# Kernel optimization log

Hardware: AMD Instinct MI355X
Metric: run time of the kernel (lower is better)

The kernel has to match this reference:

```python
import jax, jax.numpy as jnp
import numpy as np

D_MODEL = 1024
D_STATE = 32
EXPAND = 2
D_INNER = D_MODEL * EXPAND
B_SZ = 2
SEQ = 512


def setup_inputs() -> dict:
    key = jax.random.key(0)
    ks = jax.random.split(key, 10)
    x = jax.random.normal(ks[0], (B_SZ, SEQ, D_MODEL), dtype=jnp.float32)
    W_in = jax.random.normal(ks[1], (2 * D_INNER, D_MODEL), dtype=jnp.float32) * 0.02
    A_log = jax.random.uniform(ks[2], (D_INNER, D_STATE), minval=-4.0, maxval=-1.0, dtype=jnp.float32)
    W_B = jax.random.normal(ks[3], (D_STATE, D_MODEL), dtype=jnp.float32) * 0.02
    W_C = jax.random.normal(ks[4], (D_STATE, D_MODEL), dtype=jnp.float32) * 0.02
    W_dt = jax.random.normal(ks[5], (D_INNER, D_MODEL), dtype=jnp.float32) * 0.02
    b_dt = jnp.zeros((D_INNER,), dtype=jnp.float32)
    dt_bias = jnp.zeros((D_INNER,), dtype=jnp.float32) - 4.0
    rope_freq = jax.random.normal(ks[6], (D_STATE // 2,), dtype=jnp.float32) * 0.01
    ln_w = jnp.ones((D_INNER,), dtype=jnp.float32)
    ln_b = jnp.zeros((D_INNER,), dtype=jnp.float32)
    W_out = jax.random.normal(ks[7], (D_MODEL, D_INNER), dtype=jnp.float32) * 0.02
    return {"x": x, "W_in": W_in, "A_log": A_log, "W_B": W_B, "W_C": W_C,
            "W_dt": W_dt, "b_dt": b_dt, "dt_bias": dt_bias, "rope_freq": rope_freq,
            "ln_w": ln_w, "ln_b": ln_b, "W_out": W_out}


def _forward(x, W_in, A_log, W_B, W_C, W_dt, b_dt, dt_bias, rope_freq, ln_w, ln_b, W_out):
    B, L, _ = x.shape
    half = D_STATE // 2
    offset = 0

    xz = jnp.einsum('bld,ed->ble', x, W_in)                 # [B,L,2*D_INNER]
    x_inner = xz[..., :D_INNER]                             # [B,L,DI]
    z = jax.nn.silu(xz[..., D_INNER:])                      # [B,L,DI]

    A = -jnp.exp(A_log)                                     # [DI,DS]
    Bm = jnp.einsum('bld,nd->bln', x, W_B)                  # [B,L,DS]
    Cm = jnp.einsum('bld,nd->bln', x, W_C)                  # [B,L,DS]
    dt = jax.nn.softplus(jnp.einsum('bld,ed->ble', x, W_dt) + b_dt + dt_bias)  # [B,L,DI]

    # trapezoidal discretization
    dtA = dt[..., None] * A                                 # [B,L,DI,DS]
    denom = 1.0 - dtA / 2.0
    A_bar = (1.0 + dtA / 2.0) / denom                       # [B,L,DI,DS]
    B_bar = dt[..., None] / denom                           # [B,L,DI,DS]

    # per-step rope rotation angles: angle_t = rope_freq * (t + offset)
    t_idx = jnp.arange(L, dtype=jnp.float32) + offset       # [L]
    ang = t_idx[:, None] * rope_freq                        # [L,half]
    cos_a = jnp.cos(ang)
    sin_a = jnp.sin(ang)

    def step(state, inp):
        A_t, Bb_t, B_t, x_t, C_t, c_t, s_t = inp
        # state update: [B,DI,DS]
        state = A_t * state + Bb_t * B_t[:, None, :] * x_t[:, :, None]
        real = state[..., :half]
        imag = state[..., half:]
        state = jnp.concatenate([real * c_t - imag * s_t,
                                 real * s_t + imag * c_t], axis=-1)
        y_t = jnp.einsum('bds,bs->bd', state, C_t)          # [B,DI]
        return state, y_t

    state0 = jnp.zeros((B, D_INNER, D_STATE), dtype=x.dtype)
    xs = (jnp.swapaxes(A_bar, 0, 1), jnp.swapaxes(B_bar, 0, 1),
          jnp.swapaxes(Bm, 0, 1), jnp.swapaxes(x_inner, 0, 1),
          jnp.swapaxes(Cm, 0, 1), cos_a, sin_a)
    final_state, ys = jax.lax.scan(step, state0, xs)        # ys: [L,B,DI]
    out = jnp.swapaxes(ys, 0, 1) * z                        # [B,L,DI]

    # LayerNorm over last dim (eps=1e-5, torch default)
    mu = jnp.mean(out, axis=-1, keepdims=True)
    var = jnp.mean((out - mu) ** 2, axis=-1, keepdims=True)
    out = (out - mu) * jax.lax.rsqrt(var + 1e-5) * ln_w + ln_b

    out = jnp.einsum('ble,de->bld', out, W_out)             # [B,L,D_MODEL]
    return out, final_state


def reference(x, W_in, A_log, W_B, W_C, W_dt, b_dt, dt_bias, rope_freq, ln_w, ln_b, W_out):
    return _forward(x, W_in, A_log, W_B, W_C, W_dt, b_dt, dt_bias, rope_freq, ln_w, ln_b, W_out)
```

## Files before the change

### kernel.cpp

```cpp
#include <hip/hip_runtime.h>
#include <math.h>

#define B_SZ 2
#define SEQ 512
#define DM 1024
#define DI 2048
#define DS 32
#define TOK (B_SZ*SEQ)
#define NCH 8
#define CLEN (SEQ/NCH)
#define NPAIRH 32768

#define NFUSED 6272

typedef float v2f __attribute__((ext_vector_type(2)));

__device__ __forceinline__ unsigned short f2bf(float f) {
  unsigned int u = __builtin_bit_cast(unsigned int, f);
  unsigned int r = u + 0x7fffu + ((u >> 16) & 1u);
  return (unsigned short)(r >> 16);
}

template<int CTRL>
__device__ __forceinline__ float row_ror_add(float x) {
  int s = __builtin_amdgcn_update_dpp(0, __builtin_bit_cast(int, x), CTRL, 0xf, 0xf, false);
  return x + __builtin_bit_cast(float, s);
}
__device__ __forceinline__ float row16_sum(float v) {
  v = row_ror_add<0x121>(v);
  v = row_ror_add<0x122>(v);
  v = row_ror_add<0x124>(v);
  v = row_ror_add<0x128>(v);
  return v;
}

__global__ __launch_bounds__(256) void fused_cast(const float* __restrict__ x,
                                                  const float* __restrict__ W_in,
                                                  const float* __restrict__ W_dt,
                                                  const float* __restrict__ W_B,
                                                  const float* __restrict__ W_C,
                                                  const float* __restrict__ W_out,
                                                  unsigned short* __restrict__ xb,
                                                  unsigned short* __restrict__ wcat,
                                                  unsigned short* __restrict__ wob) {
  int g = blockIdx.x * 256 + threadIdx.x;
  const float* s; unsigned short* dd; int off;
  if      (g <  131072) { s = x;     dd = xb;             off = 0; }
  else if (g <  655360) { s = W_in;  dd = wcat;           off = 131072; }
  else if (g <  917504) { s = W_dt;  dd = wcat + 4194304; off = 655360; }
  else if (g <  921600) { s = W_B;   dd = wcat + 6291456; off = 917504; }
  else if (g <  925696) { s = W_C;   dd = wcat + 6324224; off = 921600; }
  else if (g < 1187840) { s = W_out; dd = wob;            off = 925696; }
  else return;
  int i = g - off;
  float4 a = ((const float4*)s)[i * 2];
  float4 b = ((const float4*)s)[i * 2 + 1];
  union { unsigned short us[8]; uint4 v; } o;
  o.us[0] = f2bf(a.x); o.us[1] = f2bf(a.y); o.us[2] = f2bf(a.z); o.us[3] = f2bf(a.w);
  o.us[4] = f2bf(b.x); o.us[5] = f2bf(b.y); o.us[6] = f2bf(b.z); o.us[7] = f2bf(b.w);
  ((uint4*)dd)[i] = o.v;
}

typedef __attribute__((ext_vector_type(8))) short  frag8;
typedef __attribute__((ext_vector_type(4))) float  facc4;

__device__ __forceinline__ void gload_lds16(const unsigned short* g, unsigned short* l) {
  __builtin_amdgcn_global_load_lds((const __attribute__((address_space(1))) unsigned int*)g,
                                   (__attribute__((address_space(3))) unsigned int*)l, 16, 0, 0);
}
__device__ __forceinline__ void gload_lds16f(const float* g, float* l) {
  __builtin_amdgcn_global_load_lds((const __attribute__((address_space(1))) unsigned int*)g,
                                   (__attribute__((address_space(3))) unsigned int*)l, 16, 0, 0);
}

__device__ __forceinline__ float softplus_fast(float v) {
  return fmaxf(v, 0.f) + __logf(1.f + __expf(-fabsf(v)));
}

template<int MT, int NT, int KSP, bool ROUTE>
__global__ __launch_bounds__(256) void gemm_mfma(const unsigned short* __restrict__ A,
                                                 const unsigned short* __restrict__ Bw,
                                                 int K,
                                                 float* __restrict__ o_xs,
                                                 float* __restrict__ o_zb,
                                                 float* __restrict__ o_dts,
                                                 float* __restrict__ o_bcb,
                                                 const float* __restrict__ b_dt,
                                                 const float* __restrict__ dt_bias,
                                                 float* __restrict__ o_c, int ldc) {
  __shared__ __align__(16) unsigned short As[64 * 64];
  __shared__ __align__(16) unsigned short Bs[64 * 64];
  const int tid = threadIdx.x;
  const int w = tid >> 6, lane = tid & 63;
  const int wm = w >> 1, wn = w & 1;
  const int bid = blockIdx.x;
  const int Wk = (bid & 7) * ((int)gridDim.x >> 3) + (bid >> 3);
  const int ks = Wk / (MT * NT);
  const int rem = Wk % (MT * NT);
  const int m0 = (rem % MT) * 64;
  const int n0 = (rem / MT) * 64;
  const int kLen = K / KSP, kBeg = ks * kLen;
  const int r = lane & 15, q = lane >> 4;
  const int srow = lane >> 3;
  const int scol = ((lane & 7) ^ (srow & 7)) * 8;
  facc4 acc[2][2] = {};
  const unsigned short* Ag = A + (size_t)m0 * K + kBeg;
  const unsigned short* Bg = Bw + (size_t)n0 * K + kBeg;

  for (int k0 = 0; k0 < kLen; k0 += 64) {
#pragma unroll
    for (int k = 0; k < 2; ++k) {
      int ch = w * 2 + k;
      gload_lds16(Ag + (size_t)(ch * 8 + srow) * K + k0 + scol, &As[ch * 512]);
      gload_lds16(Bg + (size_t)(ch * 8 + srow) * K + k0 + scol, &Bs[ch * 512]);
    }
    __syncthreads();
#pragma unroll
    for (int kk = 0; kk < 2; ++kk) {
      frag8 af[2], bf[2];
      const int sw = ((kk * 4 + q) ^ (r & 7)) * 8;
#pragma unroll
      for (int i = 0; i < 2; ++i)
        af[i] = *(const frag8*)&As[(wm * 32 + i * 16 + r) * 64 + sw];
#pragma unroll
      for (int jj = 0; jj < 2; ++jj)
        bf[jj] = *(const frag8*)&Bs[(wn * 32 + jj * 16 + r) * 64 + sw];
#pragma unroll
      for (int i = 0; i < 2; ++i)
#pragma unroll
        for (int jj = 0; jj < 2; ++jj)
          acc[i][jj] = __builtin_amdgcn_mfma_f32_16x16x32_bf16(af[i], bf[jj], acc[i][jj], 0, 0, 0);
    }
    __syncthreads();
  }

#pragma unroll
  for (int i = 0; i < 2; ++i) {
#pragma unroll
    for (int jj = 0; jj < 2; ++jj) {
      int n = n0 + wn * 32 + jj * 16 + r;
      int mb = m0 + wm * 32 + i * 16 + q * 4;
      if (ROUTE) {
        if (n < 2048) {
#pragma unroll
          for (int rg = 0; rg < 4; ++rg)
            o_xs[(size_t)(mb + rg) * DI + n] = acc[i][jj][rg];
        } else if (n < 4096) {
#pragma unroll
          for (int rg = 0; rg < 4; ++rg)
            o_zb[(size_t)(mb + rg) * DI + (n - 2048)] = acc[i][jj][rg];
        } else if (n < 6144) {
          int d = n - 4096;
          float bias = b_dt[d] + dt_bias[d];
#pragma unroll
          for (int rg = 0; rg < 4; ++rg)
            o_dts[(size_t)(mb + rg) * DI + d] = softplus_fast(acc[i][jj][rg] + bias);
        } else if (n < 6176) {
#pragma unroll
          for (int rg = 0; rg < 4; ++rg)
            o_bcb[(size_t)(mb + rg) * DS + (n - 6144)] = acc[i][jj][rg];
        } else if (n < 6208) {
#pragma unroll
          for (int rg = 0; rg < 4; ++rg)
            o_bcb[(size_t)TOK * DS + (size_t)(mb + rg) * DS + (n - 6176)] = acc[i][jj][rg];
        }
      } else {
        float* oc = o_c + (size_t)ks * (MT * 64) * ldc;
#pragma unroll
        for (int rg = 0; rg < 4; ++rg)
          oc[(size_t)(mb + rg) * ldc + n] = acc[i][jj][rg];
      }
    }
  }
}

__global__ __launch_bounds__(256) void addk(const float* __restrict__ p0,
                                            const float* __restrict__ p1,
                                            float* __restrict__ o) {
  int i = blockIdx.x * 256 + threadIdx.x;
  float4 a = ((const float4*)p0)[i];
  float4 b = ((const float4*)p1)[i];
  ((float4*)o)[i] = make_float4(a.x + b.x, a.y + b.y, a.z + b.z, a.w + b.w);
}

__global__ __launch_bounds__(256) void scan_p1(const float* __restrict__ xs,
                                               const float* __restrict__ dts,
                                               const float* __restrict__ bcb,
                                               const float* __restrict__ A_log,
                                               const float* __restrict__ rope,
                                               float* __restrict__ Pbuf) {
  __shared__ __align__(16) float lds[6144];
  const int blk = blockIdx.x;
  const int c = blk >> 7;
  const int sub = blk & 127;
  const int b = sub >> 6;
  const int dbase = (sub & 63) << 5;
  const int tid = threadIdx.x;
  const int wv = tid >> 6, lane = tid & 63;
  const int j = tid & 15;
  const int ca = (tid >> 4) & 15;
  const int l0 = c * CLEN;
  const size_t base = (size_t)(b * SEQ + l0);

  {
    int row = wv * 16 + (lane >> 3);
    int col = (lane & 7) << 2;
#pragma unroll
    for (int k = 0; k < 2; ++k) {
      gload_lds16f(xs  + (base + row + k * 8) * DI + dbase + col, &lds[(wv * 16 + k * 8) * 32]);
      gload_lds16f(dts + (base + row + k * 8) * DI + dbase + col, &lds[2048 + (wv * 16 + k * 8) * 32]);
    }
#pragma unroll
    for (int k = 0; k < 2; ++k) {
      int seg = wv * 2 + k;
      gload_lds16f(bcb + base * DS + seg * 256 + lane * 4, &lds[4096 + seg * 256]);
    }
  }

  const int dA = dbase + 2 * ca;
  v2f Ar, Ai;
  Ar.x = -0.5f * expf(A_log[dA * DS + j]);
  Ar.y = -0.5f * expf(A_log[(dA + 1) * DS + j]);
  Ai.x = -0.5f * expf(A_log[dA * DS + j + 16]);
  Ai.y = -0.5f * expf(A_log[(dA + 1) * DS + j + 16]);
  const float fr = rope[j];
  float sn, cs, sF, cF;
  sincosf((float)l0 * fr, &sn, &cs);
  sincosf(fr, &sF, &cF);
  __syncthreads();

  v2f p00 = {1.f, 1.f}, p01 = {0.f, 0.f}, p10 = {0.f, 0.f}, p11 = {1.f, 1.f};
  v2f ur = {0.f, 0.f}, ui = {0.f, 0.f};

#pragma unroll 4
  for (int tt = 0; tt < CLEN; ++tt) {
    const int ro = tt * 32;
    v2f xin = *(const v2f*)&lds[ro + 2 * ca];
    v2f dtd = *(const v2f*)&lds[2048 + ro + 2 * ca];
    float Br = lds[4096 + ro + j];
    float Bi = lds[4096 + ro + j + 16];
    v2f hr = dtd * Ar, hi = dtd * Ai;
    v2f invr, invi;
    invr.x = __builtin_amdgcn_rcpf(1.f - hr.x);
    invr.y = __builtin_amdgcn_rcpf(1.f - hr.y);
    invi.x = __builtin_amdgcn_rcpf(1.f - hi.x);
    invi.y = __builtin_amdgcn_rcpf(1.f - hi.y);
    v2f Abr = 2.f * invr - 1.f;
    v2f Abi = 2.f * invi - 1.f;
    v2f dx = dtd * xin;
    v2f bxr = dx * invr * Br;
    v2f bxi = dx * invi * Bi;
    v2f tr = Abr * ur + bxr;
    v2f ti = Abi * ui + bxi;
    ur = tr * cs - ti * sn;
    ui = tr * sn + ti * cs;
    v2f q00 = Abr * p00, q01 = Abr * p01;
    v2f q10 = Abi * p10, q11 = Abi * p11;
    p00 = q00 * cs - q10 * sn; p10 = q00 * sn + q10 * cs;
    p01 = q01 * cs - q11 * sn; p11 = q01 * sn + q11 * cs;
    float nc = fmaf(cs, cF, -sn * sF);
    float ns = fmaf(sn, cF,  cs * sF);
    cs = nc; sn = ns;
  }
  const int pc = (b * 1024 + (dbase >> 1) + ca) * 16 + j;
  float2* Pb2 = (float2*)Pbuf;
  Pb2[(c * 6 + 0) * NPAIRH + pc] = make_float2(p00.x, p00.y);
  Pb2[(c * 6 + 1) * NPAIRH + pc] = make_float2(p01.x, p01.y);
  Pb2[(c * 6 + 2) * NPAIRH + pc] = make_float2(p10.x, p10.y);
  Pb2[(c * 6 + 3) * NPAIRH + pc] = make_float2(p11.x, p11.y);
  Pb2[(c * 6 + 4) * NPAIRH + pc] = make_float2(ur.x, ur.y);
  Pb2[(c * 6 + 5) * NPAIRH + pc] = make_float2(ui.x, ui.y);
}

__global__ __launch_bounds__(256) void scan_p3(const float* __restrict__ xs,
                                               const float* __restrict__ dts,
                                               const float* __restrict__ bcb,
                                               const float* __restrict__ A_log,
                                               const float* __restrict__ rope,
                                               const float* __restrict__ Pbuf,
                                               float* __restrict__ y,
                                               float* __restrict__ fstate) {
  __shared__ __align__(16) float lds[8192];
  const int blk = blockIdx.x;
  const int c = blk >> 7;
  const int sub = blk & 127;
  const int b = sub >> 6;
  const int dbase = (sub & 63) << 5;
  const int tid = threadIdx.x;
  const int wv = tid >> 6, lane = tid & 63;
  const int j = tid & 15;
  const int ca = (tid >> 4) & 15;
  const int l0 = c * CLEN;
  const size_t base = (size_t)(b * SEQ + l0);

  {
    int row = wv * 16 + (lane >> 3);
    int col = (lane & 7) << 2;
#pragma unroll
    for (int k = 0; k < 2; ++k) {
      gload_lds16f(xs  + (base + row + k * 8) * DI + dbase + col, &lds[(wv * 16 + k * 8) * 32]);
      gload_lds16f(dts + (base + row + k * 8) * DI + dbase + col, &lds[2048 + (wv * 16 + k * 8) * 32]);
    }
#pragma unroll
    for (int k = 0; k < 2; ++k) {
      int seg = wv * 2 + k;
      gload_lds16f(bcb + base * DS + seg * 256 + lane * 4, &lds[4096 + seg * 256]);
      gload_lds16f(bcb + (size_t)TOK * DS + base * DS + seg * 256 + lane * 4, &lds[6144 + seg * 256]);
    }
  }

  const int dA = dbase + 2 * ca;
  v2f Ar, Ai;
  Ar.x = -0.5f * expf(A_log[dA * DS + j]);
  Ar.y = -0.5f * expf(A_log[(dA + 1) * DS + j]);
  Ai.x = -0.5f * expf(A_log[dA * DS + j + 16]);
  Ai.y = -0.5f * expf(A_log[(dA + 1) * DS + j + 16]);
  const float fr = rope[j];
  float sn, cs, sF, cF;
  sincosf((float)l0 * fr, &sn, &cs);
  sincosf(fr, &sF, &cF);

  const int pc = (b * 1024 + (dbase >> 1) + ca) * 16 + j;
  const float2* Pb2 = (const float2*)Pbuf;
  v2f sr = {0.f, 0.f}, si = {0.f, 0.f};
  for (int k = 0; k < c; ++k) {
    float2 f;
    f = Pb2[(k * 6 + 0) * NPAIRH + pc]; v2f p00 = {f.x, f.y};
    f = Pb2[(k * 6 + 1) * NPAIRH + pc]; v2f p01 = {f.x, f.y};
    f = Pb2[(k * 6 + 2) * NPAIRH + pc]; v2f p10 = {f.x, f.y};
    f = Pb2[(k * 6 + 3) * NPAIRH + pc]; v2f p11 = {f.x, f.y};
    f = Pb2[(k * 6 + 4) * NPAIRH + pc]; v2f ur  = {f.x, f.y};
    f = Pb2[(k * 6 + 5) * NPAIRH + pc]; v2f ui  = {f.x, f.y};
    v2f nr = p00 * sr + p01 * si + ur;
    v2f ni = p10 * sr + p11 * si + ui;
    sr = nr; si = ni;
  }
  __syncthreads();

  float* yp = y + base * DI + dA;

#pragma unroll 4
  for (int tt = 0; tt < CLEN; ++tt) {
    const int ro = tt * 32;
    v2f xin = *(const v2f*)&lds[ro + 2 * ca];
    v2f dtd = *(const v2f*)&lds[2048 + ro + 2 * ca];
    float Br = lds[4096 + ro + j];
    float Bi = lds[4096 + ro + j + 16];
    float Cr = lds[6144 + ro + j];
    float Ci = lds[6144 + ro + j + 16];
    v2f hr = dtd * Ar, hi = dtd * Ai;
    v2f invr, invi;
    invr.x = __builtin_amdgcn_rcpf(1.f - hr.x);
    invr.y = __builtin_amdgcn_rcpf(1.f - hr.y);
    invi.x = __builtin_amdgcn_rcpf(1.f - hi.x);
    invi.y = __builtin_amdgcn_rcpf(1.f - hi.y);
    v2f Abr = 2.f * invr - 1.f;
    v2f Abi = 2.f * invi - 1.f;
    v2f dx = dtd * xin;
    v2f bxr = dx * invr * Br;
    v2f bxi = dx * invi * Bi;
    v2f tr = Abr * sr + bxr;
    v2f ti = Abi * si + bxi;
    sr = tr * cs - ti * sn;
    si = tr * sn + ti * cs;
    v2f p = sr * Cr + si * Ci;
    float pA = row16_sum(p.x);
    float pB = row16_sum(p.y);
    if (j == 0) *(float2*)&yp[tt * DI] = make_float2(pA, pB);
    float nc = fmaf(cs, cF, -sn * sF);
    float ns = fmaf(sn, cF,  cs * sF);
    cs = nc; sn = ns;
  }
  if (c == NCH - 1) {
    fstate[((size_t)b * DI + dA) * DS + j]          = sr.x;
    fstate[((size_t)b * DI + dA) * DS + j + 16]     = si.x;
    fstate[((size_t)b * DI + dA + 1) * DS + j]      = sr.y;
    fstate[((size_t)b * DI + dA + 1) * DS + j + 16] = si.y;
  }
}

__global__ __launch_bounds__(256) void gate_ln(const float* __restrict__ y,
                                               const float* __restrict__ zb,
                                               const float* __restrict__ lw,
                                               const float* __restrict__ lb,
                                               unsigned short* __restrict__ o) {
  int tok = blockIdx.x;
  int t = threadIdx.x;
  float g[8];
  float sum = 0.f, sq = 0.f;
#pragma unroll
  for (int i = 0; i < 8; ++i) {
    int dd = t + i * 256;
    float yv = y[(size_t)tok * DI + dd];
    float zv = zb[(size_t)tok * DI + dd];
    float sg = zv / (1.f + __expf(-zv));
    float v = yv * sg;
    g[i] = v; sum += v; sq += v * v;
  }
#pragma unroll
  for (int off = 32; off; off >>= 1) { sum += __shfl_xor(sum, off); sq += __shfl_xor(sq, off); }
  __shared__ float rs[4], rq[4];
  int w = t >> 6;
  if ((t & 63) == 0) { rs[w] = sum; rq[w] = sq; }
  __syncthreads();
  sum = rs[0] + rs[1] + rs[2] + rs[3];
  sq  = rq[0] + rq[1] + rq[2] + rq[3];
  float mu = sum * (1.f / DI);
  float var = sq * (1.f / DI) - mu * mu;
  float rstd = rsqrtf(var + 1e-5f);
#pragma unroll
  for (int i = 0; i < 8; ++i) {
    int dd = t + i * 256;
    o[(size_t)tok * DI + dd] = f2bf((g[i] - mu) * rstd * lw[dd] + lb[dd]);
  }
}

extern "C" void kernel_launch(void* const* d_in, const int* in_sizes, int n_in,
                              void* d_out, int out_size, void* d_ws, size_t ws_size,
                              hipStream_t stream) {
  const float* x       = (const float*)d_in[0];
  const float* W_in    = (const float*)d_in[1];
  const float* A_log   = (const float*)d_in[2];
  const float* W_B     = (const float*)d_in[3];
  const float* W_C     = (const float*)d_in[4];
  const float* W_dt    = (const float*)d_in[5];
  const float* b_dt    = (const float*)d_in[6];
  const float* dt_bias = (const float*)d_in[7];
  const float* rope    = (const float*)d_in[8];
  const float* ln_w    = (const float*)d_in[9];
  const float* ln_b    = (const float*)d_in[10];
  const float* W_out   = (const float*)d_in[11];
  float* out = (float*)d_out;
  float* ws = (float*)d_ws;

  float* xs   = ws;
  float* zb   = ws + 2097152;
  float* dts  = ws + 4194304;
  float* bcb  = ws + 6291456;
  unsigned short* wob  = (unsigned short*)(ws + 6356992);
  unsigned short* xb   = (unsigned short*)(ws + 7405568);
  unsigned short* wcat = (unsigned short*)(ws + 7929856);
  float* Pbuf = ws + 7929856;
  float* yb   = ws + 11141120;
  unsigned short* lnb = (unsigned short*)(ws + 13238272);
  float* Pk   = ws;
  float* fstate = out + (size_t)TOK * DM;

  fused_cast<<<4640, 256, 0, stream>>>(x, W_in, W_dt, W_B, W_C, W_out, xb, wcat, wob);
  gemm_mfma<16, 98, 1, true><<<16 * 98, 256, 0, stream>>>(
      xb, wcat, DM, xs, zb, dts, bcb, b_dt, dt_bias, nullptr, 0);
  scan_p1<<<(NCH - 1) * 128, 256, 0, stream>>>(xs, dts, bcb, A_log, rope, Pbuf);
  scan_p3<<<NCH * 128, 256, 0, stream>>>(xs, dts, bcb, A_log, rope, Pbuf, yb, fstate);
  gate_ln<<<TOK, 256, 0, stream>>>(yb, zb, ln_w, ln_b, lnb);
  gemm_mfma<16, 16, 2, false><<<16 * 16 * 2, 256, 0, stream>>>(
      lnb, wob, DI, nullptr, nullptr, nullptr, nullptr, nullptr, nullptr, Pk, DM);
  addk<<<(TOK * DM) / 1024, 256, 0, stream>>>(Pk, Pk + (size_t)TOK * DM, out);
}
```

Measured before the change: 209.1 us.

## Replace chunked two-pass scan with single sequential double-buffered scan kernel

```diff
diff --git a/kernel.cpp b/kernel.cpp
--- a/kernel.cpp
+++ b/kernel.cpp
@@ -9,7 +9,6 @@
 #define TOK (B_SZ*SEQ)
 #define NCH 8
 #define CLEN (SEQ/NCH)
-#define NPAIRH 32768
 
 #define NFUSED 6272
 
@@ -65,10 +64,6 @@
 typedef __attribute__((ext_vector_type(4))) float  facc4;
 
 __device__ __forceinline__ void gload_lds16(const unsigned short* g, unsigned short* l) {
-  __builtin_amdgcn_global_load_lds((const __attribute__((address_space(1))) unsigned int*)g,
-                                   (__attribute__((address_space(3))) unsigned int*)l, 16, 0, 0);
-}
-__device__ __forceinline__ void gload_lds16f(const float* g, float* l) {
   __builtin_amdgcn_global_load_lds((const __attribute__((address_space(1))) unsigned int*)g,
                                    (__attribute__((address_space(3))) unsigned int*)l, 16, 0, 0);
 }
@@ -183,171 +178,49 @@
   ((float4*)o)[i] = make_float4(a.x + b.x, a.y + b.y, a.z + b.z, a.w + b.w);
 }
 
-__global__ __launch_bounds__(256) void scan_p1(const float* __restrict__ xs,
-                                               const float* __restrict__ dts,
-                                               const float* __restrict__ bcb,
-                                               const float* __restrict__ A_log,
-                                               const float* __restrict__ rope,
-                                               float* __restrict__ Pbuf) {
-  __shared__ __align__(16) float lds[6144];
-  const int blk = blockIdx.x;
-  const int c = blk >> 7;
-  const int sub = blk & 127;
-  const int b = sub >> 6;
-  const int dbase = (sub & 63) << 5;
-  const int tid = threadIdx.x;
-  const int wv = tid >> 6, lane = tid & 63;
-  const int j = tid & 15;
-  const int ca = (tid >> 4) & 15;
-  const int l0 = c * CLEN;
-  const size_t base = (size_t)(b * SEQ + l0);
-
-  {
-    int row = wv * 16 + (lane >> 3);
-    int col = (lane & 7) << 2;
-#pragma unroll
-    for (int k = 0; k < 2; ++k) {
-      gload_lds16f(xs  + (base + row + k * 8) * DI + dbase + col, &lds[(wv * 16 + k * 8) * 32]);
-      gload_lds16f(dts + (base + row + k * 8) * DI + dbase + col, &lds[2048 + (wv * 16 + k * 8) * 32]);
-    }
-#pragma unroll
-    for (int k = 0; k < 2; ++k) {
-      int seg = wv * 2 + k;
-      gload_lds16f(bcb + base * DS + seg * 256 + lane * 4, &lds[4096 + seg * 256]);
-    }
-  }
-
-  const int dA = dbase + 2 * ca;
-  v2f Ar, Ai;
-  Ar.x = -0.5f * expf(A_log[dA * DS + j]);
-  Ar.y = -0.5f * expf(A_log[(dA + 1) * DS + j]);
-  Ai.x = -0.5f * expf(A_log[dA * DS + j + 16]);
-  Ai.y = -0.5f * expf(A_log[(dA + 1) * DS + j + 16]);
-  const float fr = rope[j];
-  float sn, cs, sF, cF;
-  sincosf((float)l0 * fr, &sn, &cs);
-  sincosf(fr, &sF, &cF);
-  __syncthreads();
-
-  v2f p00 = {1.f, 1.f}, p01 = {0.f, 0.f}, p10 = {0.f, 0.f}, p11 = {1.f, 1.f};
-  v2f ur = {0.f, 0.f}, ui = {0.f, 0.f};
-
+
+__device__ __forceinline__ void scan_load_chunk(const float* __restrict__ xs,
+                                                const float* __restrict__ dts,
+                                                const float* __restrict__ bcb,
+                                                int b, int c, int dbase, int tid,
+                                                float4* pre) {
+  const size_t base = (size_t)(b * SEQ + c * CLEN);
+#pragma unroll
+  for (int k = 0; k < 2; ++k) {
+    int idx = tid * 2 + k;
+    int row = idx >> 3, c4 = (idx & 7) * 4;
+    pre[k]     = *(const float4*)(xs  + (base + row) * DI + dbase + c4);
+    pre[2 + k] = *(const float4*)(dts + (base + row) * DI + dbase + c4);
+    pre[4 + k] = ((const float4*)(bcb + base * DS))[idx];
+    pre[6 + k] = ((const float4*)(bcb + (size_t)TOK * DS + base * DS))[idx];
+  }
+}
+
+__device__ __forceinline__ void scan_write_chunk(float* __restrict__ bb, int tid,
+                                                 const float4* pre) {
+#pragma unroll
+  for (int k = 0; k < 2; ++k) {
+    int idx = tid * 2 + k;
+    *(float4*)(bb + idx * 4)        = pre[k];
+    *(float4*)(bb + 2048 + idx * 4) = pre[2 + k];
+    *(float4*)(bb + 4096 + idx * 4) = pre[4 + k];
+    *(float4*)(bb + 6144 + idx * 4) = pre[6 + k];
+  }
+}
+
+__device__ __forceinline__ void scan_chunk(const float* __restrict__ bb,
+                                           float* __restrict__ yp, int ca, int j,
+                                           v2f Ar, v2f Ai, float cF, float sF,
+                                           v2f& sr, v2f& si, float& cs, float& sn) {
 #pragma unroll 4
   for (int tt = 0; tt < CLEN; ++tt) {
     const int ro = tt * 32;
-    v2f xin = *(const v2f*)&lds[ro + 2 * ca];
-    v2f dtd = *(const v2f*)&lds[2048 + ro + 2 * ca];
-    float Br = lds[4096 + ro + j];
-    float Bi = lds[4096 + ro + j + 16];
-    v2f hr = dtd * Ar, hi = dtd * Ai;
-    v2f invr, invi;
-    invr.x = __builtin_amdgcn_rcpf(1.f - hr.x);
-    invr.y = __builtin_amdgcn_rcpf(1.f - hr.y);
-    invi.x = __builtin_amdgcn_rcpf(1.f - hi.x);
-    invi.y = __builtin_amdgcn_rcpf(1.f - hi.y);
-    v2f Abr = 2.f * invr - 1.f;
-    v2f Abi = 2.f * invi - 1.f;
-    v2f dx = dtd * xin;
-    v2f bxr = dx * invr * Br;
-    v2f bxi = dx * invi * Bi;
-    v2f tr = Abr * ur + bxr;
-    v2f ti = Abi * ui + bxi;
-    ur = tr * cs - ti * sn;
-    ui = tr * sn + ti * cs;
-    v2f q00 = Abr * p00, q01 = Abr * p01;
-    v2f q10 = Abi * p10, q11 = Abi * p11;
-    p00 = q00 * cs - q10 * sn; p10 = q00 * sn + q10 * cs;
-    p01 = q01 * cs - q11 * sn; p11 = q01 * sn + q11 * cs;
-    float nc = fmaf(cs, cF, -sn * sF);
-    float ns = fmaf(sn, cF,  cs * sF);
-    cs = nc; sn = ns;
-  }
-  const int pc = (b * 1024 + (dbase >> 1) + ca) * 16 + j;
-  float2* Pb2 = (float2*)Pbuf;
-  Pb2[(c * 6 + 0) * NPAIRH + pc] = make_float2(p00.x, p00.y);
-  Pb2[(c * 6 + 1) * NPAIRH + pc] = make_float2(p01.x, p01.y);
-  Pb2[(c * 6 + 2) * NPAIRH + pc] = make_float2(p10.x, p10.y);
-  Pb2[(c * 6 + 3) * NPAIRH + pc] = make_float2(p11.x, p11.y);
-  Pb2[(c * 6 + 4) * NPAIRH + pc] = make_float2(ur.x, ur.y);
-  Pb2[(c * 6 + 5) * NPAIRH + pc] = make_float2(ui.x, ui.y);
-}
-
-__global__ __launch_bounds__(256) void scan_p3(const float* __restrict__ xs,
-                                               const float* __restrict__ dts,
-                                               const float* __restrict__ bcb,
-                                               const float* __restrict__ A_log,
-                                               const float* __restrict__ rope,
-                                               const float* __restrict__ Pbuf,
-                                               float* __restrict__ y,
-                                               float* __restrict__ fstate) {
-  __shared__ __align__(16) float lds[8192];
-  const int blk = blockIdx.x;
-  const int c = blk >> 7;
-  const int sub = blk & 127;
-  const int b = sub >> 6;
-  const int dbase = (sub & 63) << 5;
-  const int tid = threadIdx.x;
-  const int wv = tid >> 6, lane = tid & 63;
-  const int j = tid & 15;
-  const int ca = (tid >> 4) & 15;
-  const int l0 = c * CLEN;
-  const size_t base = (size_t)(b * SEQ + l0);
-
-  {
-    int row = wv * 16 + (lane >> 3);
-    int col = (lane & 7) << 2;
-#pragma unroll
-    for (int k = 0; k < 2; ++k) {
-      gload_lds16f(xs  + (base + row + k * 8) * DI + dbase + col, &lds[(wv * 16 + k * 8) * 32]);
-      gload_lds16f(dts + (base + row + k * 8) * DI + dbase + col, &lds[2048 + (wv * 16 + k * 8) * 32]);
-    }
-#pragma unroll
-    for (int k = 0; k < 2; ++k) {
-      int seg = wv * 2 + k;
-      gload_lds16f(bcb + base * DS + seg * 256 + lane * 4, &lds[4096 + seg * 256]);
-      gload_lds16f(bcb + (size_t)TOK * DS + base * DS + seg * 256 + lane * 4, &lds[6144 + seg * 256]);
-    }
-  }
-
-  const int dA = dbase + 2 * ca;
-  v2f Ar, Ai;
-  Ar.x = -0.5f * expf(A_log[dA * DS + j]);
-  Ar.y = -0.5f * expf(A_log[(dA + 1) * DS + j]);
-  Ai.x = -0.5f * expf(A_log[dA * DS + j + 16]);
-  Ai.y = -0.5f * expf(A_log[(dA + 1) * DS + j + 16]);
-  const float fr = rope[j];
-  float sn, cs, sF, cF;
-  sincosf((float)l0 * fr, &sn, &cs);
-  sincosf(fr, &sF, &cF);
-
-  const int pc = (b * 1024 + (dbase >> 1) + ca) * 16 + j;
-  const float2* Pb2 = (const float2*)Pbuf;
-  v2f sr = {0.f, 0.f}, si = {0.f, 0.f};
-  for (int k = 0; k < c; ++k) {
-    float2 f;
-    f = Pb2[(k * 6 + 0) * NPAIRH + pc]; v2f p00 = {f.x, f.y};
-    f = Pb2[(k * 6 + 1) * NPAIRH + pc]; v2f p01 = {f.x, f.y};
-    f = Pb2[(k * 6 + 2) * NPAIRH + pc]; v2f p10 = {f.x, f.y};
-    f = Pb2[(k * 6 + 3) * NPAIRH + pc]; v2f p11 = {f.x, f.y};
-    f = Pb2[(k * 6 + 4) * NPAIRH + pc]; v2f ur  = {f.x, f.y};
-    f = Pb2[(k * 6 + 5) * NPAIRH + pc]; v2f ui  = {f.x, f.y};
-    v2f nr = p00 * sr + p01 * si + ur;
-    v2f ni = p10 * sr + p11 * si + ui;
-    sr = nr; si = ni;
-  }
-  __syncthreads();
-
-  float* yp = y + base * DI + dA;
-
-#pragma unroll 4
-  for (int tt = 0; tt < CLEN; ++tt) {
-    const int ro = tt * 32;
-    v2f xin = *(const v2f*)&lds[ro + 2 * ca];
-    v2f dtd = *(const v2f*)&lds[2048 + ro + 2 * ca];
-    float Br = lds[4096 + ro + j];
-    float Bi = lds[4096 + ro + j + 16];
-    float Cr = lds[6144 + ro + j];
-    float Ci = lds[6144 + ro + j + 16];
+    v2f xin = *(const v2f*)&bb[ro + 2 * ca];
+    v2f dtd = *(const v2f*)&bb[2048 + ro + 2 * ca];
+    float Br = bb[4096 + ro + j];
+    float Bi = bb[4096 + ro + j + 16];
+    float Cr = bb[6144 + ro + j];
+    float Ci = bb[6144 + ro + j + 16];
     v2f hr = dtd * Ar, hi = dtd * Ai;
     v2f invr, invi;
     invr.x = __builtin_amdgcn_rcpf(1.f - hr.x);
@@ -371,12 +244,56 @@
     float ns = fmaf(sn, cF,  cs * sF);
     cs = nc; sn = ns;
   }
-  if (c == NCH - 1) {
-    fstate[((size_t)b * DI + dA) * DS + j]          = sr.x;
-    fstate[((size_t)b * DI + dA) * DS + j + 16]     = si.x;
-    fstate[((size_t)b * DI + dA + 1) * DS + j]      = sr.y;
-    fstate[((size_t)b * DI + dA + 1) * DS + j + 16] = si.y;
-  }
+}
+
+__global__ __launch_bounds__(256) void scan_seq(const float* __restrict__ xs,
+                                                const float* __restrict__ dts,
+                                                const float* __restrict__ bcb,
+                                                const float* __restrict__ A_log,
+                                                const float* __restrict__ rope,
+                                                float* __restrict__ y,
+                                                float* __restrict__ fstate) {
+  __shared__ __align__(16) float lds[16384];
+  const int blk = blockIdx.x;
+  const int b = blk >> 6;
+  const int dbase = (blk & 63) << 5;
+  const int tid = threadIdx.x;
+  const int j = tid & 15;
+  const int ca = (tid >> 4) & 15;
+  const int dA = dbase + 2 * ca;
+
+  v2f Ar, Ai;
+  Ar.x = -0.5f * expf(A_log[dA * DS + j]);
+  Ar.y = -0.5f * expf(A_log[(dA + 1) * DS + j]);
+  Ai.x = -0.5f * expf(A_log[dA * DS + j + 16]);
+  Ai.y = -0.5f * expf(A_log[(dA + 1) * DS + j + 16]);
+  const float fr = rope[j];
+  float sF, cF;
+  sincosf(fr, &sF, &cF);
+  float cs = 1.f, sn = 0.f;
+  v2f sr = {0.f, 0.f}, si = {0.f, 0.f};
+
+  float4 pre[8];
+  scan_load_chunk(xs, dts, bcb, b, 0, dbase, tid, pre);
+  scan_write_chunk(lds, tid, pre);
+  __syncthreads();
+
+  for (int c = 0; c < NCH; ++c) {
+    if (c + 1 < NCH)
+      scan_load_chunk(xs, dts, bcb, b, c + 1, dbase, tid, pre);
+    float* bb = lds + (c & 1) * 8192;
+    float* yp = y + (size_t)(b * SEQ + c * CLEN) * DI + dA;
+    scan_chunk(bb, yp, ca, j, Ar, Ai, cF, sF, sr, si, cs, sn);
+    if (c + 1 < NCH) {
+      scan_write_chunk(lds + ((c + 1) & 1) * 8192, tid, pre);
+      __syncthreads();
+    }
+  }
+
+  fstate[((size_t)b * DI + dA) * DS + j]          = sr.x;
+  fstate[((size_t)b * DI + dA) * DS + j + 16]     = si.x;
+  fstate[((size_t)b * DI + dA + 1) * DS + j]      = sr.y;
+  fstate[((size_t)b * DI + dA + 1) * DS + j + 16] = si.y;
 }
 
 __global__ __launch_bounds__(256) void gate_ln(const float* __restrict__ y,
@@ -440,7 +357,6 @@
   unsigned short* wob  = (unsigned short*)(ws + 6356992);
   unsigned short* xb   = (unsigned short*)(ws + 7405568);
   unsigned short* wcat = (unsigned short*)(ws + 7929856);
-  float* Pbuf = ws + 7929856;
   float* yb   = ws + 11141120;
   unsigned short* lnb = (unsigned short*)(ws + 13238272);
   float* Pk   = ws;
@@ -449,8 +365,7 @@
   fused_cast<<<4640, 256, 0, stream>>>(x, W_in, W_dt, W_B, W_C, W_out, xb, wcat, wob);
   gemm_mfma<16, 98, 1, true><<<16 * 98, 256, 0, stream>>>(
       xb, wcat, DM, xs, zb, dts, bcb, b_dt, dt_bias, nullptr, 0);
-  scan_p1<<<(NCH - 1) * 128, 256, 0, stream>>>(xs, dts, bcb, A_log, rope, Pbuf);
-  scan_p3<<<NCH * 128, 256, 0, stream>>>(xs, dts, bcb, A_log, rope, Pbuf, yb, fstate);
+  scan_seq<<<128, 256, 0, stream>>>(xs, dts, bcb, A_log, rope, yb, fstate);
   gate_ln<<<TOK, 256, 0, stream>>>(yb, zb, ln_w, ln_b, lnb);
   gemm_mfma<16, 16, 2, false><<<16 * 16 * 2, 256, 0, stream>>>(
       lnb, wob, DI, nullptr, nullptr, nullptr, nullptr, nullptr, nullptr, Pk, DM);
```

After: 248.2 us. 18.7% more time.
